# Kernel tuning notes

Measured on AMD Instinct MI355X. Metric: run time of the kernel, lower is better.

Reference implementation:

```python
import jax, jax.numpy as jnp
import numpy as np

HIDDEN = 2048
NUM_HEADS = 16
HEAD_DIM = 128
WINDOW = 1024
ROPE_THETA = 10000.0
B, L = 1, 4096


def setup_inputs() -> dict:
    key = jax.random.key(0)
    k0, k1, k2, k3, k4 = jax.random.split(key, 5)
    s = 1.0 / np.sqrt(HIDDEN)
    return {
        "hidden_states": jax.random.normal(k0, (B, L, HIDDEN), dtype=jnp.float32),
        "wq": jax.random.normal(k1, (HIDDEN, NUM_HEADS * HEAD_DIM), dtype=jnp.float32) * s,
        "wk": jax.random.normal(k2, (HIDDEN, NUM_HEADS * HEAD_DIM), dtype=jnp.float32) * s,
        "wv": jax.random.normal(k3, (HIDDEN, NUM_HEADS * HEAD_DIM), dtype=jnp.float32) * s,
        "wo": jax.random.normal(k4, (NUM_HEADS * HEAD_DIM, HIDDEN), dtype=jnp.float32) * s,
    }


def _apply_rotary(x, cos, sin):
    # x: [B, H, L, D]; cos/sin: [L, D/2]
    d2 = x.shape[-1] // 2
    x1, x2 = x[..., :d2], x[..., d2:]
    return jnp.concatenate([x1 * cos - x2 * sin, x2 * cos + x1 * sin], axis=-1)


def reference(hidden_states, wq, wk, wv, wo):
    Bsz, Ln, _ = hidden_states.shape
    dtype = hidden_states.dtype
    scale = HEAD_DIM ** (-0.5)

    def split_heads(x):
        return x.reshape(Bsz, Ln, NUM_HEADS, HEAD_DIM).transpose(0, 2, 1, 3)

    q = split_heads(hidden_states @ wq)
    k = split_heads(hidden_states @ wk)
    v = split_heads(hidden_states @ wv)

    inv_freq = 1.0 / (ROPE_THETA ** (jnp.arange(0, HEAD_DIM, 2, dtype=jnp.float32) / HEAD_DIM))
    pos = jnp.arange(Ln, dtype=jnp.float32)
    freqs = pos[:, None] * inv_freq[None, :]  # [L, D/2]
    cos = jnp.cos(freqs).astype(dtype)
    sin = jnp.sin(freqs).astype(dtype)

    q = _apply_rotary(q, cos, sin)
    k = _apply_rotary(k, cos, sin)

    q_pos = jnp.arange(Ln)[:, None]
    k_pos = jnp.arange(Ln)[None, :]
    valid = (k_pos > q_pos - WINDOW) & (k_pos <= q_pos)  # [L, L]
    neg = jnp.finfo(dtype).min

    attn = jnp.einsum("bhqd,bhkd->bhqk", q, k) * scale
    attn = jnp.where(valid, attn, neg)
    attn = jax.nn.softmax(attn, axis=-1)
    out = jnp.einsum("bhqk,bhkd->bhqd", attn, v)
    out = out.transpose(0, 2, 1, 3).reshape(Bsz, Ln, NUM_HEADS * HEAD_DIM)
    return out @ wo
```

## Files before the change

kernel.cpp:

```cpp
#include <hip/hip_runtime.h>
#include <cstdint>
#include <cstddef>

typedef unsigned short u16;
typedef __bf16 bf16x8 __attribute__((ext_vector_type(8)));
typedef float f32x4 __attribute__((ext_vector_type(4)));
typedef unsigned short u16x8 __attribute__((ext_vector_type(8)));

#define SEQ 4096
#define HID 2048
#define NH 16
#define HD 128
#define WIN 1024

__device__ __forceinline__ float bf2f(u16 u) {
  union { unsigned int i; float f; } v; v.i = ((unsigned int)u) << 16; return v.f;
}
__device__ __forceinline__ u16 f2bf(float f) {
  union { float f; unsigned int i; } v; v.f = f;
  unsigned int r = v.i + 0x7FFFu + ((v.i >> 16) & 1u);
  return (u16)(r >> 16);
}
template<int L2R>
__device__ __forceinline__ unsigned swz(unsigned o) { return o ^ (((o >> L2R) & 7u) << 4); }

__device__ __forceinline__ void gload_lds16(const u16* g, u16* l) {
  __builtin_amdgcn_global_load_lds((const __attribute__((address_space(1))) void*)g,
                                   (__attribute__((address_space(3))) void*)l, 16, 0, 0);
}


__global__ void cast_f32_bf16(const float* __restrict__ in, u16* __restrict__ out, int n4) {
  int i = blockIdx.x * blockDim.x + threadIdx.x;
  if (i < n4) {
    float4 v = ((const float4*)in)[i];
    union { u16 u[4]; unsigned long long ll; } r;
    r.u[0] = f2bf(v.x); r.u[1] = f2bf(v.y); r.u[2] = f2bf(v.z); r.u[3] = f2bf(v.w);
    ((unsigned long long*)out)[i] = r.ll;
  }
}

__global__ void transpose_cast(const float* __restrict__ W, u16* __restrict__ Wt) {
  __shared__ float t[32][33];
  const int tx = threadIdx.x & 31, ty = threadIdx.x >> 5;
  const int x0 = blockIdx.x * 32, y0 = blockIdx.y * 32;
#pragma unroll
  for (int i = 0; i < 4; ++i)
    t[ty + i * 8][tx] = W[(size_t)(y0 + ty + i * 8) * HID + x0 + tx];
  __syncthreads();
#pragma unroll
  for (int i = 0; i < 4; ++i)
    Wt[(size_t)(x0 + ty + i * 8) * HID + y0 + tx] = f2bf(t[tx][ty + i * 8]);
}

__global__ void rope_table(float* __restrict__ ctab, float* __restrict__ stab) {
  int idx = blockIdx.x * blockDim.x + threadIdx.x;
  int pos = idx >> 6, i = idx & 63;
  float invf = expf(-(float)i * 0.14391156831212787f);
  float ang = (float)pos * invf;
  float s, c;
  sincosf(ang, &s, &c);
  ctab[idx] = c; stab[idx] = s;
}

__global__ void rope_apply(u16* __restrict__ Qb, u16* __restrict__ Kb,
                           const float* __restrict__ ctab, const float* __restrict__ stab) {
  int idx = blockIdx.x * blockDim.x + threadIdx.x;
  int pos = idx >> 10;
  int rem = idx & 1023;
  int h = rem >> 6, i = rem & 63;
  size_t base = (size_t)pos * HID + h * HD + i;
  float c = ctab[(pos << 6) + i], s = stab[(pos << 6) + i];
  float q1 = bf2f(Qb[base]), q2 = bf2f(Qb[base + 64]);
  Qb[base] = f2bf(q1 * c - q2 * s);
  Qb[base + 64] = f2bf(q2 * c + q1 * s);
  float k1 = bf2f(Kb[base]), k2 = bf2f(Kb[base + 64]);
  Kb[base] = f2bf(k1 * c - k2 * s);
  Kb[base + 64] = f2bf(k2 * c + k1 * s);
}


template<bool OUT_F32>
__device__ __forceinline__ void gemm_body(const u16* __restrict__ A, const u16* __restrict__ Bt,
                                          void* __restrict__ C,
                                          u16 (&ldsA)[2][8192], u16 (&ldsB)[2][8192]) {
  const int lane = threadIdx.x & 63;
  const int wv = threadIdx.x >> 6;
  const int wr = wv >> 1, wc = wv & 1;
  const int brow = blockIdx.y * 128;
  const int bcol = blockIdx.x * 128;
  const int K = HID, N = HID;

  const f32x4 zero = {0.f, 0.f, 0.f, 0.f};
  f32x4 acc[4][4];
#pragma unroll
  for (int m = 0; m < 4; ++m)
#pragma unroll
    for (int n = 0; n < 4; ++n) acc[m][n] = zero;

  auto stage = [&](int buf, int kt) {
    const int k0 = kt * 64;
#pragma unroll
    for (int i = 0; i < 4; ++i) {
      unsigned o = ((unsigned)(wv * 4 + i) * 64 + (unsigned)lane) * 16u;
      unsigned r = o >> 7;
      unsigned cb = swz<7>(o) & 127u;
      const size_t gcol = (size_t)k0 + (cb >> 1);
      gload_lds16(A + (size_t)(brow + r) * K + gcol, &ldsA[buf][(wv * 4 + i) * 512]);
      gload_lds16(Bt + (size_t)(bcol + r) * K + gcol, &ldsB[buf][(wv * 4 + i) * 512]);
    }
  };

  stage(0, 0);
  __syncthreads();
  int buf = 0;
  const int nt = K / 64;
  for (int kt = 0; kt < nt; ++kt) {
    if (kt + 1 < nt) stage(buf ^ 1, kt + 1);
#pragma unroll
    for (int s = 0; s < 2; ++s) {
      const unsigned kb = (unsigned)(s * 64 + ((lane >> 4) & 3) * 16);
      bf16x8 af[4], bfv[4];
#pragma unroll
      for (int m = 0; m < 4; ++m) {
        unsigned row = wr * 64 + m * 16 + (lane & 15);
        af[m] = *(const bf16x8*)((const char*)&ldsA[buf][0] + swz<7>(row * 128 + kb));
      }
#pragma unroll
      for (int n = 0; n < 4; ++n) {
        unsigned row = wc * 64 + n * 16 + (lane & 15);
        bfv[n] = *(const bf16x8*)((const char*)&ldsB[buf][0] + swz<7>(row * 128 + kb));
      }
#pragma unroll
      for (int m = 0; m < 4; ++m)
#pragma unroll
        for (int n = 0; n < 4; ++n)
          acc[m][n] = __builtin_amdgcn_mfma_f32_16x16x32_bf16(af[m], bfv[n], acc[m][n], 0, 0, 0);
    }
    __syncthreads();
    buf ^= 1;
  }

#pragma unroll
  for (int m = 0; m < 4; ++m) {
    const int rbase = brow + wr * 64 + m * 16 + ((lane >> 4) & 3) * 4;
#pragma unroll
    for (int n = 0; n < 4; ++n) {
      const int cbase = bcol + wc * 64 + n * 16 + (lane & 15);
#pragma unroll
      for (int r = 0; r < 4; ++r) {
        const size_t idx = (size_t)(rbase + r) * N + cbase;
        if (OUT_F32) ((float*)C)[idx] = acc[m][n][r];
        else ((u16*)C)[idx] = f2bf(acc[m][n][r]);
      }
    }
  }
}

__global__ __launch_bounds__(256, 2) void gemm_qkv_kernel(
    const u16* __restrict__ X, const u16* __restrict__ Wqt, const u16* __restrict__ Wkt,
    const u16* __restrict__ Wvt, u16* __restrict__ Qo, u16* __restrict__ Ko, u16* __restrict__ Vo) {
  __shared__ u16 ldsA[2][8192];
  __shared__ u16 ldsB[2][8192];
  const u16* Bt = (blockIdx.z == 0) ? Wqt : (blockIdx.z == 1) ? Wkt : Wvt;
  u16* C = (blockIdx.z == 0) ? Qo : (blockIdx.z == 1) ? Ko : Vo;
  gemm_body<false>(X, Bt, C, ldsA, ldsB);
}

__global__ __launch_bounds__(256, 2) void gemm_out_kernel(
    const u16* __restrict__ Ob, const u16* __restrict__ Wot, float* __restrict__ out) {
  __shared__ u16 ldsA[2][8192];
  __shared__ u16 ldsB[2][8192];
  gemm_body<true>(Ob, Wot, out, ldsA, ldsB);
}


__global__ __launch_bounds__(256, 2) void attn_kernel(
    const u16* __restrict__ Q, const u16* __restrict__ K,
    const u16* __restrict__ V, u16* __restrict__ O) {
  __shared__ u16 q_lds[8192];
  __shared__ u16 k_lds[8192];
  __shared__ u16 vt_lds[128 * 72];
  __shared__ u16 p_lds[4][16 * 72];

  const int lane = threadIdx.x & 63;
  const int wv = threadIdx.x >> 6;
  const int g = lane >> 4;
  const int c = lane & 15;
  const int h = blockIdx.y;
  const int q0 = blockIdx.x * 64;

#pragma unroll
  for (int i = 0; i < 4; ++i) {
    unsigned o = ((unsigned)(wv * 4 + i) * 64 + (unsigned)lane) * 16u;
    unsigned r = o >> 8;
    unsigned cb = swz<8>(o) & 255u;
    gload_lds16(Q + (size_t)(q0 + r) * HID + h * HD + (cb >> 1), &q_lds[(wv * 4 + i) * 512]);
  }
  __syncthreads();

  bf16x8 qf[4];
#pragma unroll
  for (int s = 0; s < 4; ++s) {
    unsigned row = wv * 16 + c;
    qf[s] = *(const bf16x8*)((const char*)q_lds + swz<8>(row * 256 + s * 64 + g * 16));
  }

  const f32x4 zero = {0.f, 0.f, 0.f, 0.f};
  float mrow[4], lrow[4];
  f32x4 oacc[8];
#pragma unroll
  for (int r = 0; r < 4; ++r) { mrow[r] = -3e38f; lrow[r] = 0.f; }
#pragma unroll
  for (int d = 0; d < 8; ++d) oacc[d] = zero;

  const float scale = 0.08838834764831845f;
  int t_start = q0 - WIN; if (t_start < 0) t_start = 0;

  for (int t0 = t_start; t0 <= q0; t0 += 64) {
#pragma unroll
    for (int i = 0; i < 4; ++i) {
      unsigned o = ((unsigned)(wv * 4 + i) * 64 + (unsigned)lane) * 16u;
      unsigned r = o >> 8;
      unsigned cb = swz<8>(o) & 255u;
      gload_lds16(K + (size_t)(t0 + r) * HID + h * HD + (cb >> 1), &k_lds[(wv * 4 + i) * 512]);
    }
    {
      const int key = threadIdx.x & 63;
      const int dblk = threadIdx.x >> 6;
      const u16x8* src = (const u16x8*)(V + (size_t)(t0 + key) * HID + h * HD + dblk * 32);
#pragma unroll
      for (int it = 0; it < 4; ++it) {
        u16x8 vv = src[it];
#pragma unroll
        for (int j = 0; j < 8; ++j)
          vt_lds[(dblk * 32 + it * 8 + j) * 72 + key] = vv[j];
      }
    }
    __syncthreads();

    f32x4 sa[4];
#pragma unroll
    for (int kf = 0; kf < 4; ++kf) sa[kf] = zero;
#pragma unroll
    for (int s = 0; s < 4; ++s) {
#pragma unroll
      for (int kf = 0; kf < 4; ++kf) {
        unsigned row = kf * 16 + c;
        bf16x8 kb = *(const bf16x8*)((const char*)k_lds + swz<8>(row * 256 + s * 64 + g * 16));
        sa[kf] = __builtin_amdgcn_mfma_f32_16x16x32_bf16(qf[s], kb, sa[kf], 0, 0, 0);
      }
    }

    const int qbase = q0 + wv * 16 + g * 4;
    float tmax[4] = {-3e38f, -3e38f, -3e38f, -3e38f};
#pragma unroll
    for (int kf = 0; kf < 4; ++kf) {
      const int kpos = t0 + kf * 16 + c;
#pragma unroll
      for (int r = 0; r < 4; ++r) {
        const int qp = qbase + r;
        float sv = sa[kf][r] * scale;
        const bool valid = (kpos <= qp) && (kpos > qp - WIN);
        sv = valid ? sv : -3e38f;
        sa[kf][r] = sv;
        tmax[r] = fmaxf(tmax[r], sv);
      }
    }
#pragma unroll
    for (int r = 0; r < 4; ++r) {
#pragma unroll
      for (int d = 1; d < 16; d <<= 1)
        tmax[r] = fmaxf(tmax[r], __shfl_xor(tmax[r], d, 16));
    }
    float rs[4], al[4];
#pragma unroll
    for (int r = 0; r < 4; ++r) {
      const float mn = fmaxf(mrow[r], tmax[r]);
      al[r] = __expf(mrow[r] - mn);
      mrow[r] = mn;
      rs[r] = 0.f;
    }
#pragma unroll
    for (int kf = 0; kf < 4; ++kf)
#pragma unroll
      for (int r = 0; r < 4; ++r) {
        const float sv = sa[kf][r];
        const float p = (sv < -1e37f) ? 0.f : __expf(sv - mrow[r]);
        sa[kf][r] = p;
        rs[r] += p;
      }
#pragma unroll
    for (int r = 0; r < 4; ++r) {
#pragma unroll
      for (int d = 1; d < 16; d <<= 1)
        rs[r] += __shfl_xor(rs[r], d, 16);
      lrow[r] = lrow[r] * al[r] + rs[r];
    }
#pragma unroll
    for (int df = 0; df < 8; ++df)
#pragma unroll
      for (int r = 0; r < 4; ++r)
        oacc[df][r] *= al[r];

#pragma unroll
    for (int kf = 0; kf < 4; ++kf)
#pragma unroll
      for (int r = 0; r < 4; ++r)
        p_lds[wv][(g * 4 + r) * 72 + kf * 16 + c] = f2bf(sa[kf][r]);
    __syncthreads();

#pragma unroll
    for (int s2 = 0; s2 < 2; ++s2) {
      const bf16x8 pa = *(const bf16x8*)((const char*)&p_lds[wv][0] + (c * 144 + s2 * 64 + g * 16));
#pragma unroll
      for (int df = 0; df < 8; ++df) {
        const bf16x8 vb = *(const bf16x8*)((const char*)vt_lds + ((df * 16 + c) * 144 + s2 * 64 + g * 16));
        oacc[df] = __builtin_amdgcn_mfma_f32_16x16x32_bf16(pa, vb, oacc[df], 0, 0, 0);
      }
    }
    __syncthreads();
  }

  float invl[4];
#pragma unroll
  for (int r = 0; r < 4; ++r) invl[r] = 1.f / lrow[r];
#pragma unroll
  for (int df = 0; df < 8; ++df)
#pragma unroll
    for (int r = 0; r < 4; ++r) {
      const int row = q0 + wv * 16 + g * 4 + r;
      const int col = h * HD + df * 16 + c;
      O[(size_t)row * HID + col] = f2bf(oacc[df][r] * invl[r]);
    }
}


extern "C" void kernel_launch(void* const* d_in, const int* in_sizes, int n_in,
                              void* d_out, int out_size, void* d_ws, size_t ws_size,
                              hipStream_t stream) {
  const float* hidden = (const float*)d_in[0];
  const float* wq = (const float*)d_in[1];
  const float* wk = (const float*)d_in[2];
  const float* wv = (const float*)d_in[3];
  const float* wo = (const float*)d_in[4];
  float* out = (float*)d_out;

  char* ws = (char*)d_ws;
  u16* Xb  = (u16*)ws;                 ws += (size_t)SEQ * HID * 2;
  u16* Wqt = (u16*)ws;                 ws += (size_t)HID * HID * 2;
  u16* Wkt = (u16*)ws;                 ws += (size_t)HID * HID * 2;
  u16* Wvt = (u16*)ws;                 ws += (size_t)HID * HID * 2;
  u16* Wot = (u16*)ws;                 ws += (size_t)HID * HID * 2;
  u16* Qb  = (u16*)ws;                 ws += (size_t)SEQ * HID * 2;
  u16* Kb  = (u16*)ws;                 ws += (size_t)SEQ * HID * 2;
  u16* Vb  = (u16*)ws;                 ws += (size_t)SEQ * HID * 2;
  u16* Ob  = (u16*)ws;                 ws += (size_t)SEQ * HID * 2;
  float* ctab = (float*)ws;            ws += (size_t)SEQ * 64 * 4;
  float* stab = (float*)ws;            ws += (size_t)SEQ * 64 * 4;

  cast_f32_bf16<<<(SEQ * HID / 4 + 255) / 256, 256, 0, stream>>>(hidden, Xb, SEQ * HID / 4);

  dim3 tg(64, 64);
  transpose_cast<<<tg, 256, 0, stream>>>(wq, Wqt);
  transpose_cast<<<tg, 256, 0, stream>>>(wk, Wkt);
  transpose_cast<<<tg, 256, 0, stream>>>(wv, Wvt);
  transpose_cast<<<tg, 256, 0, stream>>>(wo, Wot);

  rope_table<<<(SEQ * 64) / 256, 256, 0, stream>>>(ctab, stab);

  dim3 gq(HID / 128, SEQ / 128, 3);
  gemm_qkv_kernel<<<gq, 256, 0, stream>>>(Xb, Wqt, Wkt, Wvt, Qb, Kb, Vb);

  rope_apply<<<(SEQ * NH * 64) / 256, 256, 0, stream>>>(Qb, Kb, ctab, stab);

  dim3 ga(SEQ / 64, NH);
  attn_kernel<<<ga, 256, 0, stream>>>(Qb, Kb, Vb, Ob);

  dim3 go(HID / 128, SEQ / 128);
  gemm_out_kernel<<<go, 256, 0, stream>>>(Ob, Wot, out);
}
```

Measured before the change: 318.9 us.

## Double-buffer attention K/V tiles, lazy softmax rescale, exp2, and block swizzling

The attention kernel now double-buffers K and transposed V in LDS, prefetching the next tile while computing the current one. It drops one barrier per iteration and reuses the K buffer for the initial Q load. Softmax switches to base-2 exponentials with a prescaled factor, applies masks only on the diagonal and window-edge tiles, and skips the running-max rescale unless the max grows by more than 8. All three kernels remap block indices to group neighbouring tiles for cache locality, and the MFMA sections raise wave priority. The lazy rescale and the removed sync between writing P and reading it rely on wave-local LDS ordering, and the threshold rescale trades some numerical headroom for fewer multiplies.

```diff
diff --git a/kernel.cpp b/kernel.cpp
--- a/kernel.cpp
+++ b/kernel.cpp
@@ -20,6 +20,12 @@
   union { float f; unsigned int i; } v; v.f = f;
   unsigned int r = v.i + 0x7FFFu + ((v.i >> 16) & 1u);
   return (u16)(r >> 16);
+}
+__device__ __forceinline__ u16 f2bf_rne(float f) {
+  union { __bf16 b; u16 u; } v; v.b = (__bf16)f; return v.u;
+}
+__device__ __forceinline__ float exp2a(float x) {
+  float r; asm("v_exp_f32 %0, %1" : "=v"(r) : "v"(x)); return r;
 }
 template<int L2R>
 __device__ __forceinline__ unsigned swz(unsigned o) { return o ^ (((o >> L2R) & 7u) << 4); }
@@ -82,13 +88,11 @@
 
 template<bool OUT_F32>
 __device__ __forceinline__ void gemm_body(const u16* __restrict__ A, const u16* __restrict__ Bt,
-                                          void* __restrict__ C,
+                                          void* __restrict__ C, int brow, int bcol,
                                           u16 (&ldsA)[2][8192], u16 (&ldsB)[2][8192]) {
   const int lane = threadIdx.x & 63;
   const int wv = threadIdx.x >> 6;
   const int wr = wv >> 1, wc = wv & 1;
-  const int brow = blockIdx.y * 128;
-  const int bcol = blockIdx.x * 128;
   const int K = HID, N = HID;
 
   const f32x4 zero = {0.f, 0.f, 0.f, 0.f};
@@ -117,6 +121,7 @@
   const int nt = K / 64;
   for (int kt = 0; kt < nt; ++kt) {
     if (kt + 1 < nt) stage(buf ^ 1, kt + 1);
+    __builtin_amdgcn_s_setprio(1);
 #pragma unroll
     for (int s = 0; s < 2; ++s) {
       const unsigned kb = (unsigned)(s * 64 + ((lane >> 4) & 3) * 16);
@@ -137,6 +142,7 @@
         for (int n = 0; n < 4; ++n)
           acc[m][n] = __builtin_amdgcn_mfma_f32_16x16x32_bf16(af[m], bfv[n], acc[m][n], 0, 0, 0);
     }
+    __builtin_amdgcn_s_setprio(0);
     __syncthreads();
     buf ^= 1;
   }
@@ -162,164 +168,233 @@
     const u16* __restrict__ Wvt, u16* __restrict__ Qo, u16* __restrict__ Ko, u16* __restrict__ Vo) {
   __shared__ u16 ldsA[2][8192];
   __shared__ u16 ldsB[2][8192];
-  const u16* Bt = (blockIdx.z == 0) ? Wqt : (blockIdx.z == 1) ? Wkt : Wvt;
-  u16* C = (blockIdx.z == 0) ? Qo : (blockIdx.z == 1) ? Ko : Vo;
-  gemm_body<false>(X, Bt, C, ldsA, ldsB);
+  int flat = (blockIdx.z * 32 + blockIdx.y) * 16 + blockIdx.x;
+  int nf = (flat & 7) * 192 + (flat >> 3);
+  int bx = nf & 15, by = (nf >> 4) & 31, bz = nf >> 9;
+  const u16* Bt = (bz == 0) ? Wqt : (bz == 1) ? Wkt : Wvt;
+  u16* C = (bz == 0) ? Qo : (bz == 1) ? Ko : Vo;
+  gemm_body<false>(X, Bt, C, by * 128, bx * 128, ldsA, ldsB);
 }
 
 __global__ __launch_bounds__(256, 2) void gemm_out_kernel(
     const u16* __restrict__ Ob, const u16* __restrict__ Wot, float* __restrict__ out) {
   __shared__ u16 ldsA[2][8192];
   __shared__ u16 ldsB[2][8192];
-  gemm_body<true>(Ob, Wot, out, ldsA, ldsB);
+  int flat = blockIdx.y * 16 + blockIdx.x;
+  int nf = (flat & 7) * 64 + (flat >> 3);
+  int bx = nf & 15, by = nf >> 4;
+  gemm_body<true>(Ob, Wot, out, by * 128, bx * 128, ldsA, ldsB);
 }
 
 
 __global__ __launch_bounds__(256, 2) void attn_kernel(
     const u16* __restrict__ Q, const u16* __restrict__ K,
     const u16* __restrict__ V, u16* __restrict__ O) {
-  __shared__ u16 q_lds[8192];
-  __shared__ u16 k_lds[8192];
-  __shared__ u16 vt_lds[128 * 72];
+  __shared__ u16 k_lds[2][8192];
+  __shared__ u16 vt_lds[2][128 * 72];
   __shared__ u16 p_lds[4][16 * 72];
 
   const int lane = threadIdx.x & 63;
   const int wv = threadIdx.x >> 6;
   const int g = lane >> 4;
   const int c = lane & 15;
-  const int h = blockIdx.y;
-  const int q0 = blockIdx.x * 64;
+
+  int flat = blockIdx.y * 64 + blockIdx.x;
+  int nf = (flat & 7) * 128 + (flat >> 3);
+  const int q0 = (nf & 63) * 64;
+  const int h = nf >> 6;
 
 #pragma unroll
   for (int i = 0; i < 4; ++i) {
     unsigned o = ((unsigned)(wv * 4 + i) * 64 + (unsigned)lane) * 16u;
     unsigned r = o >> 8;
     unsigned cb = swz<8>(o) & 255u;
-    gload_lds16(Q + (size_t)(q0 + r) * HID + h * HD + (cb >> 1), &q_lds[(wv * 4 + i) * 512]);
+    gload_lds16(Q + (size_t)(q0 + r) * HID + h * HD + (cb >> 1), &k_lds[0][(wv * 4 + i) * 512]);
   }
   __syncthreads();
-
   bf16x8 qf[4];
 #pragma unroll
   for (int s = 0; s < 4; ++s) {
     unsigned row = wv * 16 + c;
-    qf[s] = *(const bf16x8*)((const char*)q_lds + swz<8>(row * 256 + s * 64 + g * 16));
-  }
+    qf[s] = *(const bf16x8*)((const char*)&k_lds[0][0] + swz<8>(row * 256 + s * 64 + g * 16));
+  }
+  __syncthreads();
+
+  const int t_start = (q0 >= WIN) ? (q0 - WIN) : 0;
+
+#pragma unroll
+  for (int i = 0; i < 4; ++i) {
+    unsigned o = ((unsigned)(wv * 4 + i) * 64 + (unsigned)lane) * 16u;
+    unsigned r = o >> 8;
+    unsigned cb = swz<8>(o) & 255u;
+    gload_lds16(K + (size_t)(t_start + r) * HID + h * HD + (cb >> 1), &k_lds[0][(wv * 4 + i) * 512]);
+  }
+  {
+    const u16x8* src = (const u16x8*)(V + (size_t)(t_start + lane) * HID + h * HD + wv * 32);
+#pragma unroll
+    for (int it = 0; it < 4; ++it) {
+      u16x8 vv = src[it];
+#pragma unroll
+      for (int j = 0; j < 8; ++j)
+        vt_lds[0][(wv * 32 + it * 8 + j) * 72 + lane] = vv[j];
+    }
+  }
+  __syncthreads();
 
   const f32x4 zero = {0.f, 0.f, 0.f, 0.f};
   float mrow[4], lrow[4];
   f32x4 oacc[8];
 #pragma unroll
-  for (int r = 0; r < 4; ++r) { mrow[r] = -3e38f; lrow[r] = 0.f; }
+  for (int r = 0; r < 4; ++r) { mrow[r] = -1e30f; lrow[r] = 0.f; }
 #pragma unroll
   for (int d = 0; d < 8; ++d) oacc[d] = zero;
 
-  const float scale = 0.08838834764831845f;
-  int t_start = q0 - WIN; if (t_start < 0) t_start = 0;
+  const float scale2 = 0.12751743f;
+  int b = 0;
 
   for (int t0 = t_start; t0 <= q0; t0 += 64) {
-#pragma unroll
-    for (int i = 0; i < 4; ++i) {
-      unsigned o = ((unsigned)(wv * 4 + i) * 64 + (unsigned)lane) * 16u;
-      unsigned r = o >> 8;
-      unsigned cb = swz<8>(o) & 255u;
-      gload_lds16(K + (size_t)(t0 + r) * HID + h * HD + (cb >> 1), &k_lds[(wv * 4 + i) * 512]);
-    }
-    {
-      const int key = threadIdx.x & 63;
-      const int dblk = threadIdx.x >> 6;
-      const u16x8* src = (const u16x8*)(V + (size_t)(t0 + key) * HID + h * HD + dblk * 32);
-#pragma unroll
-      for (int it = 0; it < 4; ++it) {
-        u16x8 vv = src[it];
-#pragma unroll
-        for (int j = 0; j < 8; ++j)
-          vt_lds[(dblk * 32 + it * 8 + j) * 72 + key] = vv[j];
-      }
-    }
-    __syncthreads();
+    const int nb = b ^ 1;
+    const bool has_next = (t0 + 64 <= q0);
+
+    u16x8 vreg[4];
+    if (has_next) {
+#pragma unroll
+      for (int i = 0; i < 4; ++i) {
+        unsigned o = ((unsigned)(wv * 4 + i) * 64 + (unsigned)lane) * 16u;
+        unsigned r = o >> 8;
+        unsigned cb = swz<8>(o) & 255u;
+        gload_lds16(K + (size_t)(t0 + 64 + r) * HID + h * HD + (cb >> 1),
+                    &k_lds[nb][(wv * 4 + i) * 512]);
+      }
+      const u16x8* src = (const u16x8*)(V + (size_t)(t0 + 64 + lane) * HID + h * HD + wv * 32);
+#pragma unroll
+      for (int it = 0; it < 4; ++it) vreg[it] = src[it];
+    }
 
     f32x4 sa[4];
 #pragma unroll
     for (int kf = 0; kf < 4; ++kf) sa[kf] = zero;
+    __builtin_amdgcn_s_setprio(1);
 #pragma unroll
     for (int s = 0; s < 4; ++s) {
 #pragma unroll
       for (int kf = 0; kf < 4; ++kf) {
         unsigned row = kf * 16 + c;
-        bf16x8 kb = *(const bf16x8*)((const char*)k_lds + swz<8>(row * 256 + s * 64 + g * 16));
+        bf16x8 kb = *(const bf16x8*)((const char*)&k_lds[b][0] + swz<8>(row * 256 + s * 64 + g * 16));
         sa[kf] = __builtin_amdgcn_mfma_f32_16x16x32_bf16(qf[s], kb, sa[kf], 0, 0, 0);
       }
     }
+    __builtin_amdgcn_s_setprio(0);
 
     const int qbase = q0 + wv * 16 + g * 4;
-    float tmax[4] = {-3e38f, -3e38f, -3e38f, -3e38f};
-#pragma unroll
-    for (int kf = 0; kf < 4; ++kf) {
-      const int kpos = t0 + kf * 16 + c;
-#pragma unroll
-      for (int r = 0; r < 4; ++r) {
-        const int qp = qbase + r;
-        float sv = sa[kf][r] * scale;
-        const bool valid = (kpos <= qp) && (kpos > qp - WIN);
-        sv = valid ? sv : -3e38f;
-        sa[kf][r] = sv;
-        tmax[r] = fmaxf(tmax[r], sv);
-      }
-    }
-#pragma unroll
-    for (int r = 0; r < 4; ++r) {
+    const bool diag = (t0 == q0);
+    const bool lowm = (q0 >= WIN) && (t0 == t_start);
+    if (diag) {
+#pragma unroll
+      for (int kf = 0; kf < 4; ++kf) {
+        const int kpos = t0 + kf * 16 + c;
+#pragma unroll
+        for (int r = 0; r < 4; ++r) {
+          float x = sa[kf][r] * scale2;
+          sa[kf][r] = (kpos <= qbase + r) ? x : -1e30f;
+        }
+      }
+    } else if (lowm) {
+#pragma unroll
+      for (int kf = 0; kf < 4; ++kf) {
+        const int kpos = t0 + kf * 16 + c;
+#pragma unroll
+        for (int r = 0; r < 4; ++r) {
+          float x = sa[kf][r] * scale2;
+          sa[kf][r] = (kpos > qbase + r - WIN) ? x : -1e30f;
+        }
+      }
+    } else {
+#pragma unroll
+      for (int kf = 0; kf < 4; ++kf)
+#pragma unroll
+        for (int r = 0; r < 4; ++r) sa[kf][r] *= scale2;
+    }
+
+    float tmax[4];
+#pragma unroll
+    for (int r = 0; r < 4; ++r)
+      tmax[r] = fmaxf(fmaxf(sa[0][r], sa[1][r]), fmaxf(sa[2][r], sa[3][r]));
+#pragma unroll
+    for (int r = 0; r < 4; ++r)
 #pragma unroll
       for (int d = 1; d < 16; d <<= 1)
         tmax[r] = fmaxf(tmax[r], __shfl_xor(tmax[r], d, 16));
-    }
-    float rs[4], al[4];
+
+    bool okl = (tmax[0] <= mrow[0] + 8.f) && (tmax[1] <= mrow[1] + 8.f) &&
+               (tmax[2] <= mrow[2] + 8.f) && (tmax[3] <= mrow[3] + 8.f);
+    if (!__all((int)okl)) {
+#pragma unroll
+      for (int r = 0; r < 4; ++r) {
+        const float mn = fmaxf(mrow[r], tmax[r]);
+        const float al = exp2a(mrow[r] - mn);
+        mrow[r] = mn;
+        lrow[r] *= al;
+#pragma unroll
+        for (int df = 0; df < 8; ++df) oacc[df][r] *= al;
+      }
+    }
+
+    float rs[4] = {0.f, 0.f, 0.f, 0.f};
+    if (diag || lowm) {
+#pragma unroll
+      for (int kf = 0; kf < 4; ++kf)
+#pragma unroll
+        for (int r = 0; r < 4; ++r) {
+          const float x = sa[kf][r];
+          const float p = (x < -1e29f) ? 0.f : exp2a(x - mrow[r]);
+          sa[kf][r] = p; rs[r] += p;
+        }
+    } else {
+#pragma unroll
+      for (int kf = 0; kf < 4; ++kf)
+#pragma unroll
+        for (int r = 0; r < 4; ++r) {
+          const float p = exp2a(sa[kf][r] - mrow[r]);
+          sa[kf][r] = p; rs[r] += p;
+        }
+    }
 #pragma unroll
     for (int r = 0; r < 4; ++r) {
-      const float mn = fmaxf(mrow[r], tmax[r]);
-      al[r] = __expf(mrow[r] - mn);
-      mrow[r] = mn;
-      rs[r] = 0.f;
-    }
+#pragma unroll
+      for (int d = 1; d < 16; d <<= 1) rs[r] += __shfl_xor(rs[r], d, 16);
+      lrow[r] += rs[r];
+    }
+
 #pragma unroll
     for (int kf = 0; kf < 4; ++kf)
 #pragma unroll
-      for (int r = 0; r < 4; ++r) {
-        const float sv = sa[kf][r];
-        const float p = (sv < -1e37f) ? 0.f : __expf(sv - mrow[r]);
-        sa[kf][r] = p;
-        rs[r] += p;
-      }
-#pragma unroll
-    for (int r = 0; r < 4; ++r) {
-#pragma unroll
-      for (int d = 1; d < 16; d <<= 1)
-        rs[r] += __shfl_xor(rs[r], d, 16);
-      lrow[r] = lrow[r] * al[r] + rs[r];
-    }
-#pragma unroll
-    for (int df = 0; df < 8; ++df)
-#pragma unroll
       for (int r = 0; r < 4; ++r)
-        oacc[df][r] *= al[r];
-
-#pragma unroll
-    for (int kf = 0; kf < 4; ++kf)
-#pragma unroll
-      for (int r = 0; r < 4; ++r)
-        p_lds[wv][(g * 4 + r) * 72 + kf * 16 + c] = f2bf(sa[kf][r]);
-    __syncthreads();
-
+        p_lds[wv][(g * 4 + r) * 72 + kf * 16 + c] = f2bf_rne(sa[kf][r]);
+
+    if (has_next) {
+#pragma unroll
+      for (int it = 0; it < 4; ++it)
+#pragma unroll
+        for (int j = 0; j < 8; ++j)
+          vt_lds[nb][(wv * 32 + it * 8 + j) * 72 + lane] = vreg[it][j];
+    }
+
+    asm volatile("" ::: "memory");
+
+    __builtin_amdgcn_s_setprio(1);
 #pragma unroll
     for (int s2 = 0; s2 < 2; ++s2) {
       const bf16x8 pa = *(const bf16x8*)((const char*)&p_lds[wv][0] + (c * 144 + s2 * 64 + g * 16));
 #pragma unroll
       for (int df = 0; df < 8; ++df) {
-        const bf16x8 vb = *(const bf16x8*)((const char*)vt_lds + ((df * 16 + c) * 144 + s2 * 64 + g * 16));
+        const bf16x8 vb = *(const bf16x8*)((const char*)&vt_lds[b][0] + ((df * 16 + c) * 144 + s2 * 64 + g * 16));
         oacc[df] = __builtin_amdgcn_mfma_f32_16x16x32_bf16(pa, vb, oacc[df], 0, 0, 0);
       }
     }
+    __builtin_amdgcn_s_setprio(0);
     __syncthreads();
+    b = nb;
   }
 
   float invl[4];
```

Measured after the change: 300.5 us. 1.06x faster.
